# Optimization experiments

Hardware: AMD Instinct MI355X
Metric: run time of the kernel (lower is better)

## Reference

```python
import jax, jax.numpy as jnp
import numpy as np

EMBED_DIM = 256
NUM_HEADS = 8
HEAD_DIM = EMBED_DIM // NUM_HEADS
ADJ_CHANNELS = 4
B, N = 8, 1024


def setup_inputs() -> dict:
    key = jax.random.key(0)
    ks = jax.random.split(key, 12)
    s = 1.0 / np.sqrt(EMBED_DIM)
    sa = 1.0 / np.sqrt(ADJ_CHANNELS)
    return {
        "x": jax.random.normal(ks[0], (B, N, EMBED_DIM), dtype=jnp.float32),
        "adj": jax.random.uniform(ks[1], (B, N, N, ADJ_CHANNELS), dtype=jnp.float32),
        "Wq": jax.random.uniform(ks[2], (EMBED_DIM, EMBED_DIM), jnp.float32, -s, s),
        "bq": jnp.zeros((EMBED_DIM,), jnp.float32),
        "Wk": jax.random.uniform(ks[3], (EMBED_DIM, EMBED_DIM), jnp.float32, -s, s),
        "bk": jnp.zeros((EMBED_DIM,), jnp.float32),
        "Wv": jax.random.uniform(ks[4], (EMBED_DIM, EMBED_DIM), jnp.float32, -s, s),
        "bv": jnp.zeros((EMBED_DIM,), jnp.float32),
        "Wo": jax.random.uniform(ks[5], (EMBED_DIM, EMBED_DIM), jnp.float32, -s, s),
        "bo": jnp.zeros((EMBED_DIM,), jnp.float32),
        "Wa": jax.random.uniform(ks[6], (ADJ_CHANNELS, NUM_HEADS), jnp.float32, -sa, sa),
        "ba": jnp.zeros((NUM_HEADS,), jnp.float32),
    }


def reference(x, adj, Wq, bq, Wk, bk, Wv, bv, Wo, bo, Wa, ba):
    Bs, Ns, E = x.shape
    H, D = NUM_HEADS, HEAD_DIM
    def heads(W, b):
        return (x @ W + b).reshape(Bs, Ns, H, D).transpose(0, 2, 1, 3)  # [B,H,N,D]
    Q, K, V = heads(Wq, bq), heads(Wk, bk), heads(Wv, bv)
    # adjacency-derived additive bias: [B,N,N,C] -> [B,N,N,H] -> [B,H,N,N]
    bias = jnp.moveaxis(adj @ Wa + ba, -1, 1)
    scores = jnp.einsum("bhnd,bhmd->bhnm", Q, K) / np.sqrt(D) + bias
    attn = jax.nn.softmax(scores, axis=-1)
    ctx = jnp.einsum("bhnm,bhmd->bhnd", attn, V)  # [B,H,N,D]
    ctx = ctx.transpose(0, 2, 1, 3).reshape(Bs, Ns, E)
    return ctx @ Wo + bo + x
```

## Files before the change

### kernel.cpp

```cpp
#include <hip/hip_runtime.h>
#include <hip/hip_bf16.h>

#define BATCH 8
#define SEQ   1024
#define EMB   256
#define NH    8
#define HD    32
#define QSCALE 0.2550030053f

typedef __attribute__((ext_vector_type(8))) short short8;
typedef __attribute__((ext_vector_type(4))) float floatx4;

__device__ __forceinline__ ushort f2bf(float f) {
    __hip_bfloat16 h = __float2bfloat16(f);
    return *reinterpret_cast<ushort*>(&h);
}

__device__ __forceinline__ void gload_lds16(const float4* g, float4* l) {
    __builtin_amdgcn_global_load_lds(
        (const __attribute__((address_space(1))) unsigned int*)g,
        (__attribute__((address_space(3))) unsigned int*)l, 16, 0, 0);
}

__global__ __launch_bounds__(256) void prep_kernel(
    const float* __restrict__ Wq, const float* __restrict__ Wk,
    const float* __restrict__ Wv, const float* __restrict__ Wo,
    ushort* __restrict__ Wqt, ushort* __restrict__ Wkt,
    ushort* __restrict__ Wvt, ushort* __restrict__ Wot)
{
    __shared__ float tilebuf[32][33];
    const int blk = blockIdx.x;
    const int mat = blk >> 6, tile = blk & 63;
    const int ti = tile >> 3, tj = tile & 7;
    const float* W = (mat == 0) ? Wq : (mat == 1) ? Wk : (mat == 2) ? Wv : Wo;
    ushort* Wt = (mat == 0) ? Wqt : (mat == 1) ? Wkt : (mat == 2) ? Wvt : Wot;
    const float scale = (mat == 0) ? QSCALE : 1.0f;

    const int tx = threadIdx.x & 31, ty = threadIdx.x >> 5;
    #pragma unroll
    for (int p = 0; p < 4; ++p)
        tilebuf[ty + p * 8][tx] = W[(size_t)(ti * 32 + ty + p * 8) * EMB + tj * 32 + tx];
    __syncthreads();
    #pragma unroll
    for (int p = 0; p < 4; ++p)
        Wt[(size_t)(tj * 32 + ty + p * 8) * EMB + ti * 32 + tx] =
            f2bf(tilebuf[tx][ty + p * 8] * scale);
}

__global__ __launch_bounds__(256) void qkv_gemm(
    const float* __restrict__ x,
    const ushort* __restrict__ Wqt, const ushort* __restrict__ Wkt,
    const ushort* __restrict__ Wvt,
    const float* __restrict__ bq, const float* __restrict__ bk,
    const float* __restrict__ bv,
    ushort* __restrict__ Qb, ushort* __restrict__ Kb, ushort* __restrict__ Vt)
{
    const int mat = blockIdx.y;
    const ushort* __restrict__ Wt = (mat == 0) ? Wqt : (mat == 1) ? Wkt : Wvt;
    const float* __restrict__ bias = (mat == 0) ? bq : (mat == 1) ? bk : bv;
    const float bscale = (mat == 0) ? QSCALE : 1.0f;

    const int w = threadIdx.x >> 6, lane = threadIdx.x & 63;
    const int quad = lane >> 4, l16 = lane & 15;
    const int row0 = blockIdx.x * 64 + w * 16;

    floatx4 acc[16];
    #pragma unroll
    for (int i = 0; i < 16; ++i) acc[i] = (floatx4){0.f, 0.f, 0.f, 0.f};

    const float* __restrict__ xrow = x + (size_t)(row0 + l16) * EMB + quad * 8;

    #pragma unroll
    for (int ks = 0; ks < 8; ++ks) {
        const float4 xa0 = *(const float4*)(xrow + ks * 32);
        const float4 xa1 = *(const float4*)(xrow + ks * 32 + 4);
        ushort au[8] = {f2bf(xa0.x), f2bf(xa0.y), f2bf(xa0.z), f2bf(xa0.w),
                        f2bf(xa1.x), f2bf(xa1.y), f2bf(xa1.z), f2bf(xa1.w)};
        const short8 a = *(const short8*)au;
        #pragma unroll
        for (int i = 0; i < 16; ++i) {
            const short8 bf = *(const short8*)(Wt + (size_t)(i * 16 + l16) * EMB + ks * 32 + quad * 8);
            acc[i] = __builtin_amdgcn_mfma_f32_16x16x32_bf16(a, bf, acc[i], 0, 0, 0);
        }
    }

    const int gr0 = row0 + quad * 4;
    if (mat < 2) {
        ushort* __restrict__ dst = (mat == 0) ? Qb : Kb;
        #pragma unroll
        for (int i = 0; i < 16; ++i) {
            const int c = i * 16 + l16, h = c >> 5, d = c & (HD - 1);
            const float bb = bias[c] * bscale;
            #pragma unroll
            for (int r = 0; r < 4; ++r) {
                const int gr = gr0 + r, b = gr >> 10, n = gr & (SEQ - 1);
                dst[((size_t)(b * NH + h) * SEQ + n) * HD + d] = f2bf(acc[i][r] + bb);
            }
        }
    } else {
        const int b = gr0 >> 10, n0 = gr0 & (SEQ - 1);
        #pragma unroll
        for (int i = 0; i < 16; ++i) {
            const int c = i * 16 + l16, h = c >> 5, d = c & (HD - 1);
            const float bb = bias[c];
            ushort4 t4;
            t4.x = f2bf(acc[i][0] + bb); t4.y = f2bf(acc[i][1] + bb);
            t4.z = f2bf(acc[i][2] + bb); t4.w = f2bf(acc[i][3] + bb);
            *(ushort4*)(Vt + ((size_t)(b * NH + h) * HD + d) * SEQ + n0) = t4;
        }
    }
}

__global__ __launch_bounds__(512) void attn_kernel(
    const ushort* __restrict__ Qb, const ushort* __restrict__ Kb,
    const ushort* __restrict__ Vt, const float* __restrict__ adj,
    const float* __restrict__ Wa, const float* __restrict__ ba,
    float* __restrict__ cp, float* __restrict__ lsum)
{
    __shared__ float4 Atile[2][16][65];
    __shared__ ushort Plds[NH][2][16][36];
    const int tid = threadIdx.x, h = tid >> 6, lane = tid & 63;
    const int quad = lane >> 4, l16 = lane & 15;
    const int q0 = blockIdx.x * 16, b = blockIdx.y, z = blockIdx.z;
    const int bh = b * NH + h;
    const int kz = z * 512;

    const float LOG2E = 1.4426950408889634f;
    const float wa0 = Wa[0 * NH + h] * LOG2E, wa1 = Wa[1 * NH + h] * LOG2E;
    const float wa2 = Wa[2 * NH + h] * LOG2E, wa3 = Wa[3 * NH + h] * LOG2E;
    const float bah = ba[h] * LOG2E;

    const short8 aq = *(const short8*)(Qb + ((size_t)bh * SEQ + q0 + l16) * HD + quad * 8);

    floatx4 o0 = {0.f, 0.f, 0.f, 0.f}, o1 = {0.f, 0.f, 0.f, 0.f};
    float lrow[4] = {0.f, 0.f, 0.f, 0.f};

    const float4* __restrict__ adjb = (const float4*)adj + (size_t)b * SEQ * SEQ;
    const float4* __restrict__ asrc0 = adjb + (size_t)(q0 + 2 * h)     * SEQ + kz + lane;
    const float4* __restrict__ asrc1 = adjb + (size_t)(q0 + 2 * h + 1) * SEQ + kz + lane;

    const ushort* __restrict__ Kbase = Kb + (size_t)bh * SEQ * HD + (size_t)l16 * HD + quad * 8;
    const ushort* __restrict__ Vb0 = Vt + ((size_t)bh * HD + l16) * SEQ + quad * 8;
    const ushort* __restrict__ Vb1 = Vt + ((size_t)bh * HD + 16 + l16) * SEQ + quad * 8;

    gload_lds16(asrc0, &Atile[0][2 * h][0]);
    gload_lds16(asrc1, &Atile[0][2 * h + 1][0]);
    __syncthreads();

    for (int it = 0; it < 8; ++it) {
        const int cur = it & 1;
        const int key0 = kz + it * 64;

        if (it < 7) {
            gload_lds16(asrc0 + (it + 1) * 64, &Atile[cur ^ 1][2 * h][0]);
            gload_lds16(asrc1 + (it + 1) * 64, &Atile[cur ^ 1][2 * h + 1][0]);
        }

        const short8 k0 = *(const short8*)(Kbase + (size_t)(key0)      * HD);
        const short8 k1 = *(const short8*)(Kbase + (size_t)(key0 + 16) * HD);
        const short8 k2 = *(const short8*)(Kbase + (size_t)(key0 + 32) * HD);
        const short8 k3 = *(const short8*)(Kbase + (size_t)(key0 + 48) * HD);
        const floatx4 zz = {0.f, 0.f, 0.f, 0.f};
        floatx4 s0 = __builtin_amdgcn_mfma_f32_16x16x32_bf16(aq, k0, zz, 0, 0, 0);
        floatx4 s1 = __builtin_amdgcn_mfma_f32_16x16x32_bf16(aq, k1, zz, 0, 0, 0);
        floatx4 s2 = __builtin_amdgcn_mfma_f32_16x16x32_bf16(aq, k2, zz, 0, 0, 0);
        floatx4 s3 = __builtin_amdgcn_mfma_f32_16x16x32_bf16(aq, k3, zz, 0, 0, 0);

        #pragma unroll
        for (int r = 0; r < 4; ++r) {
            const int row = quad * 4 + r;
            const float4 a0 = Atile[cur][row][l16];
            const float4 a1 = Atile[cur][row][16 + l16];
            const float4 a2 = Atile[cur][row][32 + l16];
            const float4 a3 = Atile[cur][row][48 + l16];
            const float b0 = fmaf(a0.x, wa0, fmaf(a0.y, wa1, fmaf(a0.z, wa2, fmaf(a0.w, wa3, bah))));
            const float b1 = fmaf(a1.x, wa0, fmaf(a1.y, wa1, fmaf(a1.z, wa2, fmaf(a1.w, wa3, bah))));
            const float b2 = fmaf(a2.x, wa0, fmaf(a2.y, wa1, fmaf(a2.z, wa2, fmaf(a2.w, wa3, bah))));
            const float b3 = fmaf(a3.x, wa0, fmaf(a3.y, wa1, fmaf(a3.z, wa2, fmaf(a3.w, wa3, bah))));
            const float p0 = exp2f(s0[r] + b0);
            const float p1 = exp2f(s1[r] + b1);
            const float p2 = exp2f(s2[r] + b2);
            const float p3 = exp2f(s3[r] + b3);
            lrow[r] += (p0 + p1) + (p2 + p3);
            Plds[h][0][row][l16]      = f2bf(p0);
            Plds[h][0][row][16 + l16] = f2bf(p1);
            Plds[h][1][row][l16]      = f2bf(p2);
            Plds[h][1][row][16 + l16] = f2bf(p3);
        }
        __builtin_amdgcn_s_waitcnt(0xc07f);

        const short8 ap0 = *(const short8*)&Plds[h][0][l16][quad * 8];
        const short8 ap1 = *(const short8*)&Plds[h][1][l16][quad * 8];
        const short8 v0 = *(const short8*)(Vb0 + key0);
        const short8 v1 = *(const short8*)(Vb1 + key0);
        const short8 v2 = *(const short8*)(Vb0 + key0 + 32);
        const short8 v3 = *(const short8*)(Vb1 + key0 + 32);
        o0 = __builtin_amdgcn_mfma_f32_16x16x32_bf16(ap0, v0, o0, 0, 0, 0);
        o1 = __builtin_amdgcn_mfma_f32_16x16x32_bf16(ap0, v1, o1, 0, 0, 0);
        o0 = __builtin_amdgcn_mfma_f32_16x16x32_bf16(ap1, v2, o0, 0, 0, 0);
        o1 = __builtin_amdgcn_mfma_f32_16x16x32_bf16(ap1, v3, o1, 0, 0, 0);

        __syncthreads();
    }

    #pragma unroll
    for (int r = 0; r < 4; ++r) {
        lrow[r] += __shfl_xor(lrow[r], 1, 64);
        lrow[r] += __shfl_xor(lrow[r], 2, 64);
        lrow[r] += __shfl_xor(lrow[r], 4, 64);
        lrow[r] += __shfl_xor(lrow[r], 8, 64);
    }

    float* __restrict__ cpz = cp + (size_t)z * BATCH * SEQ * EMB;
    float* __restrict__ lsz = lsum + (size_t)z * BATCH * SEQ * NH;
    #pragma unroll
    for (int r = 0; r < 4; ++r) {
        const size_t grow = (size_t)b * SEQ + q0 + quad * 4 + r;
        cpz[grow * EMB + h * HD + l16]      = o0[r];
        cpz[grow * EMB + h * HD + 16 + l16] = o1[r];
        if (l16 == 0) lsz[grow * NH + h] = lrow[r];
    }
}

__global__ __launch_bounds__(256) void outproj_gemm(
    const float* __restrict__ cp, const float* __restrict__ lsum,
    const ushort* __restrict__ Wot, const float* __restrict__ bo,
    const float* __restrict__ x, float* __restrict__ out)
{
    const int w = threadIdx.x >> 6, lane = threadIdx.x & 63;
    const int quad = lane >> 4, l16 = lane & 15;
    const int row0 = blockIdx.x * 64 + w * 16;
    const int arow = row0 + l16;
    const float* __restrict__ cp1 = cp + (size_t)BATCH * SEQ * EMB;
    const float* __restrict__ l1  = lsum + (size_t)BATCH * SEQ * NH;

    floatx4 acc[16];
    #pragma unroll
    for (int i = 0; i < 16; ++i) acc[i] = (floatx4){0.f, 0.f, 0.f, 0.f};

    #pragma unroll
    for (int ks = 0; ks < 8; ++ks) {
        const float invl = 1.0f / (lsum[(size_t)arow * NH + ks] + l1[(size_t)arow * NH + ks]);
        const size_t cb = (size_t)arow * EMB + ks * 32 + quad * 8;
        const float4 c00 = *(const float4*)(cp + cb);
        const float4 c01 = *(const float4*)(cp + cb + 4);
        const float4 c10 = *(const float4*)(cp1 + cb);
        const float4 c11 = *(const float4*)(cp1 + cb + 4);
        ushort au[8] = {
            f2bf((c00.x + c10.x) * invl), f2bf((c00.y + c10.y) * invl),
            f2bf((c00.z + c10.z) * invl), f2bf((c00.w + c10.w) * invl),
            f2bf((c01.x + c11.x) * invl), f2bf((c01.y + c11.y) * invl),
            f2bf((c01.z + c11.z) * invl), f2bf((c01.w + c11.w) * invl)};
        const short8 a = *(const short8*)au;
        #pragma unroll
        for (int i = 0; i < 16; ++i) {
            const short8 bfr = *(const short8*)(Wot + (size_t)(i * 16 + l16) * EMB + ks * 32 + quad * 8);
            acc[i] = __builtin_amdgcn_mfma_f32_16x16x32_bf16(a, bfr, acc[i], 0, 0, 0);
        }
    }

    const int gr0 = row0 + quad * 4;
    #pragma unroll
    for (int i = 0; i < 16; ++i) {
        const int c = i * 16 + l16;
        const float bov = bo[c];
        #pragma unroll
        for (int r = 0; r < 4; ++r) {
            const size_t idx = (size_t)(gr0 + r) * EMB + c;
            out[idx] = acc[i][r] + bov + x[idx];
        }
    }
}

extern "C" void kernel_launch(void* const* d_in, const int* in_sizes, int n_in,
                              void* d_out, int out_size, void* d_ws, size_t ws_size,
                              hipStream_t stream) {
    const float* x   = (const float*)d_in[0];
    const float* adj = (const float*)d_in[1];
    const float* Wq  = (const float*)d_in[2];
    const float* bq  = (const float*)d_in[3];
    const float* Wk  = (const float*)d_in[4];
    const float* bk  = (const float*)d_in[5];
    const float* Wv  = (const float*)d_in[6];
    const float* bv  = (const float*)d_in[7];
    const float* Wo  = (const float*)d_in[8];
    const float* bo  = (const float*)d_in[9];
    const float* Wa  = (const float*)d_in[10];
    const float* ba  = (const float*)d_in[11];

    const size_t per = (size_t)BATCH * NH * SEQ * HD;
    ushort* Qb  = (ushort*)d_ws;
    ushort* Kb  = Qb + per;
    ushort* Vt  = Kb + per;
    ushort* Wqt = Vt + per;
    ushort* Wkt = Wqt + EMB * EMB;
    ushort* Wvt = Wkt + EMB * EMB;
    ushort* Wot = Wvt + EMB * EMB;
    float*  cp  = (float*)(Wot + EMB * EMB);
    float*  ls  = cp + 2 * (size_t)BATCH * SEQ * EMB;

    prep_kernel<<<256, 256, 0, stream>>>(Wq, Wk, Wv, Wo, Wqt, Wkt, Wvt, Wot);
    qkv_gemm<<<dim3(BATCH * SEQ / 64, 3), 256, 0, stream>>>(
        x, Wqt, Wkt, Wvt, bq, bk, bv, Qb, Kb, Vt);
    attn_kernel<<<dim3(SEQ / 16, BATCH, 2), 512, 0, stream>>>(
        Qb, Kb, Vt, adj, Wa, ba, cp, ls);
    outproj_gemm<<<BATCH * SEQ / 64, 256, 0, stream>>>(
        cp, ls, Wot, bo, x, (float*)d_out);
}
```

Baseline: 298.7 us.

## Transpose score MFMA to keep P in registers and split outproj columns

```diff
diff --git a/kernel.cpp b/kernel.cpp
--- a/kernel.cpp
+++ b/kernel.cpp
@@ -99,6 +99,10 @@
         }
     } else {
         const int b = gr0 >> 10, n0 = gr0 & (SEQ - 1);
+        const int j0 = n0 & 31;
+        const int slot = (j0 < 16) ? ((j0 >> 2) << 3)
+                                   : ((((j0 - 16) >> 2) << 3) + 4);
+        const int nperm = (n0 & ~31) | slot;
         #pragma unroll
         for (int i = 0; i < 16; ++i) {
             const int c = i * 16 + l16, h = c >> 5, d = c & (HD - 1);
@@ -106,7 +110,7 @@
             ushort4 t4;
             t4.x = f2bf(acc[i][0] + bb); t4.y = f2bf(acc[i][1] + bb);
             t4.z = f2bf(acc[i][2] + bb); t4.w = f2bf(acc[i][3] + bb);
-            *(ushort4*)(Vt + ((size_t)(b * NH + h) * HD + d) * SEQ + n0) = t4;
+            *(ushort4*)(Vt + ((size_t)(b * NH + h) * HD + d) * SEQ + nperm) = t4;
         }
     }
 }
@@ -118,7 +122,6 @@
     float* __restrict__ cp, float* __restrict__ lsum)
 {
     __shared__ float4 Atile[2][16][65];
-    __shared__ ushort Plds[NH][2][16][36];
     const int tid = threadIdx.x, h = tid >> 6, lane = tid & 63;
     const int quad = lane >> 4, l16 = lane & 15;
     const int q0 = blockIdx.x * 16, b = blockIdx.y, z = blockIdx.z;
@@ -133,7 +136,7 @@
     const short8 aq = *(const short8*)(Qb + ((size_t)bh * SEQ + q0 + l16) * HD + quad * 8);
 
     floatx4 o0 = {0.f, 0.f, 0.f, 0.f}, o1 = {0.f, 0.f, 0.f, 0.f};
-    float lrow[4] = {0.f, 0.f, 0.f, 0.f};
+    float lacc = 0.f;
 
     const float4* __restrict__ adjb = (const float4*)adj + (size_t)b * SEQ * SEQ;
     const float4* __restrict__ asrc0 = adjb + (size_t)(q0 + 2 * h)     * SEQ + kz + lane;
@@ -161,18 +164,19 @@
         const short8 k2 = *(const short8*)(Kbase + (size_t)(key0 + 32) * HD);
         const short8 k3 = *(const short8*)(Kbase + (size_t)(key0 + 48) * HD);
         const floatx4 zz = {0.f, 0.f, 0.f, 0.f};
-        floatx4 s0 = __builtin_amdgcn_mfma_f32_16x16x32_bf16(aq, k0, zz, 0, 0, 0);
-        floatx4 s1 = __builtin_amdgcn_mfma_f32_16x16x32_bf16(aq, k1, zz, 0, 0, 0);
-        floatx4 s2 = __builtin_amdgcn_mfma_f32_16x16x32_bf16(aq, k2, zz, 0, 0, 0);
-        floatx4 s3 = __builtin_amdgcn_mfma_f32_16x16x32_bf16(aq, k3, zz, 0, 0, 0);
-
+        floatx4 s0 = __builtin_amdgcn_mfma_f32_16x16x32_bf16(k0, aq, zz, 0, 0, 0);
+        floatx4 s1 = __builtin_amdgcn_mfma_f32_16x16x32_bf16(k1, aq, zz, 0, 0, 0);
+        floatx4 s2 = __builtin_amdgcn_mfma_f32_16x16x32_bf16(k2, aq, zz, 0, 0, 0);
+        floatx4 s3 = __builtin_amdgcn_mfma_f32_16x16x32_bf16(k3, aq, zz, 0, 0, 0);
+
+        ushort pu0[8], pu1[8];
         #pragma unroll
         for (int r = 0; r < 4; ++r) {
-            const int row = quad * 4 + r;
-            const float4 a0 = Atile[cur][row][l16];
-            const float4 a1 = Atile[cur][row][16 + l16];
-            const float4 a2 = Atile[cur][row][32 + l16];
-            const float4 a3 = Atile[cur][row][48 + l16];
+            const int col = 4 * quad + r;
+            const float4 a0 = Atile[cur][l16][col];
+            const float4 a1 = Atile[cur][l16][16 + col];
+            const float4 a2 = Atile[cur][l16][32 + col];
+            const float4 a3 = Atile[cur][l16][48 + col];
             const float b0 = fmaf(a0.x, wa0, fmaf(a0.y, wa1, fmaf(a0.z, wa2, fmaf(a0.w, wa3, bah))));
             const float b1 = fmaf(a1.x, wa0, fmaf(a1.y, wa1, fmaf(a1.z, wa2, fmaf(a1.w, wa3, bah))));
             const float b2 = fmaf(a2.x, wa0, fmaf(a2.y, wa1, fmaf(a2.z, wa2, fmaf(a2.w, wa3, bah))));
@@ -181,45 +185,36 @@
             const float p1 = exp2f(s1[r] + b1);
             const float p2 = exp2f(s2[r] + b2);
             const float p3 = exp2f(s3[r] + b3);
-            lrow[r] += (p0 + p1) + (p2 + p3);
-            Plds[h][0][row][l16]      = f2bf(p0);
-            Plds[h][0][row][16 + l16] = f2bf(p1);
-            Plds[h][1][row][l16]      = f2bf(p2);
-            Plds[h][1][row][16 + l16] = f2bf(p3);
-        }
-        __builtin_amdgcn_s_waitcnt(0xc07f);
-
-        const short8 ap0 = *(const short8*)&Plds[h][0][l16][quad * 8];
-        const short8 ap1 = *(const short8*)&Plds[h][1][l16][quad * 8];
-        const short8 v0 = *(const short8*)(Vb0 + key0);
-        const short8 v1 = *(const short8*)(Vb1 + key0);
-        const short8 v2 = *(const short8*)(Vb0 + key0 + 32);
-        const short8 v3 = *(const short8*)(Vb1 + key0 + 32);
-        o0 = __builtin_amdgcn_mfma_f32_16x16x32_bf16(ap0, v0, o0, 0, 0, 0);
-        o1 = __builtin_amdgcn_mfma_f32_16x16x32_bf16(ap0, v1, o1, 0, 0, 0);
-        o0 = __builtin_amdgcn_mfma_f32_16x16x32_bf16(ap1, v2, o0, 0, 0, 0);
-        o1 = __builtin_amdgcn_mfma_f32_16x16x32_bf16(ap1, v3, o1, 0, 0, 0);
+            lacc += (p0 + p1) + (p2 + p3);
+            pu0[r]     = f2bf(p0);
+            pu0[4 + r] = f2bf(p1);
+            pu1[r]     = f2bf(p2);
+            pu1[4 + r] = f2bf(p3);
+        }
+        const short8 pf0 = *(const short8*)pu0;
+        const short8 pf1 = *(const short8*)pu1;
+
+        const short8 v00 = *(const short8*)(Vb0 + key0);
+        const short8 v10 = *(const short8*)(Vb1 + key0);
+        const short8 v01 = *(const short8*)(Vb0 + key0 + 32);
+        const short8 v11 = *(const short8*)(Vb1 + key0 + 32);
+        o0 = __builtin_amdgcn_mfma_f32_16x16x32_bf16(v00, pf0, o0, 0, 0, 0);
+        o1 = __builtin_amdgcn_mfma_f32_16x16x32_bf16(v10, pf0, o1, 0, 0, 0);
+        o0 = __builtin_amdgcn_mfma_f32_16x16x32_bf16(v01, pf1, o0, 0, 0, 0);
+        o1 = __builtin_amdgcn_mfma_f32_16x16x32_bf16(v11, pf1, o1, 0, 0, 0);
 
         __syncthreads();
     }
 
-    #pragma unroll
-    for (int r = 0; r < 4; ++r) {
-        lrow[r] += __shfl_xor(lrow[r], 1, 64);
-        lrow[r] += __shfl_xor(lrow[r], 2, 64);
-        lrow[r] += __shfl_xor(lrow[r], 4, 64);
-        lrow[r] += __shfl_xor(lrow[r], 8, 64);
-    }
+    lacc += __shfl_xor(lacc, 16, 64);
+    lacc += __shfl_xor(lacc, 32, 64);
 
     float* __restrict__ cpz = cp + (size_t)z * BATCH * SEQ * EMB;
     float* __restrict__ lsz = lsum + (size_t)z * BATCH * SEQ * NH;
-    #pragma unroll
-    for (int r = 0; r < 4; ++r) {
-        const size_t grow = (size_t)b * SEQ + q0 + quad * 4 + r;
-        cpz[grow * EMB + h * HD + l16]      = o0[r];
-        cpz[grow * EMB + h * HD + 16 + l16] = o1[r];
-        if (l16 == 0) lsz[grow * NH + h] = lrow[r];
-    }
+    const size_t grow = (size_t)b * SEQ + q0 + l16;
+    *(floatx4*)(cpz + grow * EMB + h * HD + 4 * quad)      = o0;
+    *(floatx4*)(cpz + grow * EMB + h * HD + 16 + 4 * quad) = o1;
+    if (quad == 0) lsz[grow * NH + h] = lacc;
 }
 
 __global__ __launch_bounds__(256) void outproj_gemm(
@@ -230,13 +225,14 @@
     const int w = threadIdx.x >> 6, lane = threadIdx.x & 63;
     const int quad = lane >> 4, l16 = lane & 15;
     const int row0 = blockIdx.x * 64 + w * 16;
+    const int c0 = blockIdx.y * 128;
     const int arow = row0 + l16;
     const float* __restrict__ cp1 = cp + (size_t)BATCH * SEQ * EMB;
     const float* __restrict__ l1  = lsum + (size_t)BATCH * SEQ * NH;
 
-    floatx4 acc[16];
-    #pragma unroll
-    for (int i = 0; i < 16; ++i) acc[i] = (floatx4){0.f, 0.f, 0.f, 0.f};
+    floatx4 acc[8];
+    #pragma unroll
+    for (int i = 0; i < 8; ++i) acc[i] = (floatx4){0.f, 0.f, 0.f, 0.f};
 
     #pragma unroll
     for (int ks = 0; ks < 8; ++ks) {
@@ -253,16 +249,16 @@
             f2bf((c01.z + c11.z) * invl), f2bf((c01.w + c11.w) * invl)};
         const short8 a = *(const short8*)au;
         #pragma unroll
-        for (int i = 0; i < 16; ++i) {
-            const short8 bfr = *(const short8*)(Wot + (size_t)(i * 16 + l16) * EMB + ks * 32 + quad * 8);
+        for (int i = 0; i < 8; ++i) {
+            const short8 bfr = *(const short8*)(Wot + (size_t)(c0 + i * 16 + l16) * EMB + ks * 32 + quad * 8);
             acc[i] = __builtin_amdgcn_mfma_f32_16x16x32_bf16(a, bfr, acc[i], 0, 0, 0);
         }
     }
 
     const int gr0 = row0 + quad * 4;
     #pragma unroll
-    for (int i = 0; i < 16; ++i) {
-        const int c = i * 16 + l16;
+    for (int i = 0; i < 8; ++i) {
+        const int c = c0 + i * 16 + l16;
         const float bov = bo[c];
         #pragma unroll
         for (int r = 0; r < 4; ++r) {
@@ -304,6 +300,6 @@
         x, Wqt, Wkt, Wvt, bq, bk, bv, Qb, Kb, Vt);
     attn_kernel<<<dim3(SEQ / 16, BATCH, 2), 512, 0, stream>>>(
         Qb, Kb, Vt, adj, Wa, ba, cp, ls);
-    outproj_gemm<<<BATCH * SEQ / 64, 256, 0, stream>>>(
+    outproj_gemm<<<dim3(BATCH * SEQ / 64, 2), 256, 0, stream>>>(
         cp, ls, Wot, bo, x, (float*)d_out);
 }
```

After: 287.9 us. 1.04x faster.
